# Kernel tuning notes

Measured on AMD Instinct MI355X. Metric: run time of the kernel, lower is better.

## Reference

```python
import jax, jax.numpy as jnp
import numpy as np

B, S, VOCAB, HID, NCLS = 64, 512, 1400, 256, 128


def _time_lstm(W_all, b_all, U_all, b_u, W_d, b_d, x, ts):
    # x: [b, s, h], ts: [b, s]
    b = x.shape[0]
    h0 = jnp.zeros((b, HID), x.dtype)
    c0 = jnp.zeros((b, HID), x.dtype)

    def step(carry, xt):
        h, c = carry
        x_t, t_t = xt  # [b,h], [b]
        c_s1 = jnp.tanh(c @ W_d.T + b_d)
        c_adj = (c - c_s1) + c_s1 * t_t[:, None]
        gates = jax.nn.sigmoid(h @ W_all.T + b_all + x_t @ U_all.T + b_u)
        f, i, o, c_tmp = jnp.split(gates, 4, axis=1)  # note: c_tmp is sigmoid, as in source
        c_new = f * c_adj + i * c_tmp
        h_new = o * jnp.tanh(c_new)
        return (h_new, c_new), h_new

    _, hs = jax.lax.scan(step, (h0, c0), (x.transpose(1, 0, 2), ts.T))
    return hs.transpose(1, 0, 2)  # [b, s, h]


def setup_inputs() -> dict:
    key = jax.random.key(0)
    ks = jax.random.split(key, 18)

    def g(k, shape, scale=0.05):
        return jax.random.normal(k, shape, dtype=jnp.float32) * scale

    return {
        "inputs": jax.random.uniform(ks[0], (B, S, VOCAB), dtype=jnp.float32),
        "timestamps": jax.random.uniform(ks[1], (B, S), dtype=jnp.float32),
        "emb": g(ks[2], (VOCAB, HID)),
        "W_all1": g(ks[3], (4 * HID, HID)), "b_all1": g(ks[4], (4 * HID,)),
        "U_all1": g(ks[5], (4 * HID, HID)), "b_u1": g(ks[6], (4 * HID,)),
        "W_d1": g(ks[7], (HID, HID)), "b_d1": g(ks[8], (HID,)),
        "W_all2": g(ks[9], (4 * HID, HID)), "b_all2": g(ks[10], (4 * HID,)),
        "U_all2": g(ks[11], (4 * HID, HID)), "b_u2": g(ks[12], (4 * HID,)),
        "W_d2": g(ks[13], (HID, HID)), "b_d2": g(ks[14], (HID,)),
        "wa": g(ks[15], (1, HID)),
        "Wb": g(ks[16], (HID, HID)),
        "W_out": g(ks[17], (NCLS, HID)),
    }


def reference(inputs, timestamps, emb, W_all1, b_all1, U_all1, b_u1, W_d1, b_d1,
              W_all2, b_all2, U_all2, b_u2, W_d2, b_d2, wa, Wb, W_out):
    embedded = jnp.einsum('bsv,vh->bsh', inputs, emb)  # multi-hot embedding lookup
    out1 = _time_lstm(W_all1, b_all1, U_all1, b_u1, W_d1, b_d1, embedded, timestamps)
    out2 = _time_lstm(W_all2, b_all2, U_all2, b_u2, W_d2, b_d2, embedded, timestamps)
    alpha = jax.nn.softmax(jnp.einsum('bsh,oh->bs', out1, wa), axis=1)  # [b,s]
    Beta = jnp.tanh(jnp.einsum('bsh,gh->bsg', out2, Wb))  # [b,s,h]
    ctx = jnp.sum(embedded * Beta * alpha[:, :, None], axis=1)  # [b,h]
    return ctx @ W_out.T  # [b, num_classes]
```

## Files before the change

kernel.cpp:

```cpp
#include <hip/hip_runtime.h>

typedef __attribute__((ext_vector_type(8))) short short8;
typedef __attribute__((ext_vector_type(4))) float f32x4;

#define B_   64
#define S_   512
#define V_   1400
#define VP_  1408
#define H_   256
#define G4_  1024
#define NC_  128
#define CH_  64

__device__ __forceinline__ unsigned short f2bf(float f) {
    unsigned u = __builtin_bit_cast(unsigned, f);
    u += 0x7FFFu + ((u >> 16) & 1u);
    return (unsigned short)(u >> 16);
}
__device__ __forceinline__ float bf2f(unsigned short h) {
    unsigned u = ((unsigned)h) << 16;
    return __builtin_bit_cast(float, u);
}
__device__ __forceinline__ float fsig(float x) {
    x = fminf(fmaxf(x, -40.f), 40.f);
    float e = __builtin_amdgcn_exp2f(x * -1.44269504f);
    return __builtin_amdgcn_rcpf(1.0f + e);
}
__device__ __forceinline__ float ftanh(float x) {
    x = fminf(fmaxf(x, -40.f), 40.f);
    float e = __builtin_amdgcn_exp2f(x * 2.88539008f);
    return 1.0f - 2.0f * __builtin_amdgcn_rcpf(e + 1.0f);
}

__device__ __forceinline__ short8 gload16_sc1(const unsigned short* p) {
    short8 r;
    asm volatile("global_load_dwordx4 %0, %1, off sc1"
                 : "=v"(r) : "v"((unsigned long long)p));
    return r;
}
__device__ __forceinline__ void gstore_short_sc1(unsigned short* p, unsigned v) {
    asm volatile("global_store_short %0, %1, off sc1"
                 :: "v"((unsigned long long)p), "v"(v));
}

__global__ void k0_prep(const float* __restrict__ emb,
                        const float* __restrict__ Wa1, const float* __restrict__ Wa2,
                        const float* __restrict__ Wd1, const float* __restrict__ Wd2,
                        const float* __restrict__ U1,  const float* __restrict__ U2,
                        const float* __restrict__ ba1, const float* __restrict__ bu1,
                        const float* __restrict__ ba2, const float* __restrict__ bu2,
                        const float* __restrict__ Wb,
                        unsigned short* __restrict__ embT, unsigned short* __restrict__ Wg,
                        unsigned short* __restrict__ Wd,   unsigned short* __restrict__ Ub,
                        unsigned short* __restrict__ Wbb,  float* __restrict__ bg,
                        unsigned int* __restrict__ cnt) {
    int tid = blockIdx.x * blockDim.x + threadIdx.x;
    int np = gridDim.x * blockDim.x;
    for (int i = tid; i < 256 * VP_; i += np) {
        int n = i / VP_, k = i - n * VP_;
        embT[i] = (k < V_) ? f2bf(emb[k * H_ + n]) : (unsigned short)0;
    }
    for (int i = tid; i < G4_ * H_; i += np) {
        Wg[i] = f2bf(Wa1[i]); Wg[G4_ * H_ + i] = f2bf(Wa2[i]);
        Ub[i] = f2bf(U1[i]);  Ub[G4_ * H_ + i] = f2bf(U2[i]);
    }
    for (int i = tid; i < H_ * H_; i += np) {
        Wd[i] = f2bf(Wd1[i]); Wd[H_ * H_ + i] = f2bf(Wd2[i]); Wbb[i] = f2bf(Wb[i]);
    }
    for (int i = tid; i < G4_; i += np) {
        bg[i] = ba1[i] + bu1[i]; bg[G4_ + i] = ba2[i] + bu2[i];
    }
    for (int i = tid; i < 512; i += np) cnt[i] = 0;
}

__global__ __launch_bounds__(512, 2) void k1_embed(const float* __restrict__ inputs,
                                                   const unsigned short* __restrict__ embT,
                                                   unsigned short* __restrict__ embB) {
    const int tid = threadIdx.x;
    const int w = tid >> 6, ln = tid & 63, q = ln >> 4, l16 = ln & 15;
    const int mt = w >> 2, ng = (w & 3) * 4;
    const int Rbase = blockIdx.x * 32 + mt * 16;
    const float* arow = inputs + (long)(Rbase + l16) * V_;

    f32x4 acc[4];
    #pragma unroll
    for (int i = 0; i < 4; ++i) acc[i] = (f32x4){0.f, 0.f, 0.f, 0.f};

    for (int kt = 0; kt < 44; ++kt) {
        int k0 = kt * 32 + q * 8;
        short8 af;
        if (kt == 43 && q == 3) {
            #pragma unroll
            for (int j = 0; j < 8; ++j) af[j] = 0;
        } else {
            f32x4 x0 = *(const f32x4*)(arow + k0);
            f32x4 x1 = *(const f32x4*)(arow + k0 + 4);
            #pragma unroll
            for (int j = 0; j < 4; ++j) { af[j] = (short)f2bf(x0[j]); af[4 + j] = (short)f2bf(x1[j]); }
        }
        #pragma unroll
        for (int i = 0; i < 4; ++i) {
            short8 bf = *(const short8*)(embT + (long)((ng + i) * 16 + l16) * VP_ + k0);
            acc[i] = __builtin_amdgcn_mfma_f32_16x16x32_bf16(af, bf, acc[i], 0, 0, 0);
        }
    }
    #pragma unroll
    for (int i = 0; i < 4; ++i) {
        int col = (ng + i) * 16 + l16;
        #pragma unroll
        for (int j = 0; j < 4; ++j) {
            int R = Rbase + 4 * q + j;
            embB[(long)R * H_ + col] = f2bf(acc[i][j]);
        }
    }
}

__global__ __launch_bounds__(512, 2) void k2_pre(const unsigned short* __restrict__ embB,
                                                 const unsigned short* __restrict__ Ub,
                                                 const float* __restrict__ bg,
                                                 float* __restrict__ P, int t0) {
    const int tid = threadIdx.x;
    const int w = tid >> 6, ln = tid & 63, q = ln >> 4, l16 = ln & 15;
    const int rbase = blockIdx.x * 32;

    short8 af[2][8];
    #pragma unroll
    for (int mt = 0; mt < 2; ++mt)
        #pragma unroll
        for (int kt = 0; kt < 8; ++kt) {
            int rp = rbase + mt * 16 + l16;
            int rg = t0 * 64 + rp;
            int b = rg & 63, s = rg >> 6;
            af[mt][kt] = *(const short8*)(embB + ((long)b * S_ + s) * H_ + kt * 32 + q * 8);
        }

    for (int i = 0; i < 16; ++i) {
        int nt2 = w * 16 + i;
        int l = nt2 >> 6;
        int gcol = (nt2 & 63) * 16 + l16;
        float bias = bg[nt2 * 16 + l16];
        short8 bf[8];
        #pragma unroll
        for (int kt = 0; kt < 8; ++kt)
            bf[kt] = *(const short8*)(Ub + (long)(nt2 * 16 + l16) * H_ + kt * 32 + q * 8);
        #pragma unroll
        for (int mt = 0; mt < 2; ++mt) {
            f32x4 acc = (f32x4){bias, bias, bias, bias};
            #pragma unroll
            for (int kt = 0; kt < 8; ++kt)
                acc = __builtin_amdgcn_mfma_f32_16x16x32_bf16(af[mt][kt], bf[kt], acc, 0, 0, 0);
            int rp0 = rbase + mt * 16;
            float* dst = P + ((long)l * (CH_ * 64) + rp0 + 4 * q) * G4_ + gcol;
            #pragma unroll
            for (int j = 0; j < 4; ++j) dst[(long)j * G4_] = acc[j];
        }
    }
}

__global__ __launch_bounds__(256, 1) void k3_lstm(const float* __restrict__ ts,
                                                  const unsigned short* __restrict__ W,
                                                  const float* __restrict__ bd1,
                                                  const float* __restrict__ bd2,
                                                  const float* __restrict__ P,
                                                  unsigned short* __restrict__ out1,
                                                  unsigned short* __restrict__ out2,
                                                  float* __restrict__ cst,
                                                  unsigned short* __restrict__ cx,
                                                  unsigned int* __restrict__ cnt,
                                                  int t0) {
    __shared__ float ts_lds[16][CH_];

    const int tid = threadIdx.x;
    const int w = tid >> 6, ln = tid & 63, q = ln >> 4, l16 = ln & 15;
    const int bid = blockIdx.x;
    const int l = bid >> 4, m = (bid >> 2) & 3, cg = bid & 3;
    const int b0 = m * 16;
    const int hc0 = cg * 64 + w * 16;
    const int mycol = hc0 + l16;
    const int cidx = (l * 4 + m) * 64;
    unsigned short* outp = l ? out2 : out1;
    const float bdv = (l ? bd2 : bd1)[mycol];

    for (int i = tid; i < 16 * CH_; i += 256) {
        int r = i >> 6, cc = i & (CH_ - 1);
        ts_lds[r][cc] = ts[(b0 + r) * S_ + t0 + cc];
    }

    short8 wg[4][8];
    short8 wd[8];
    #pragma unroll
    for (int g = 0; g < 4; ++g)
        #pragma unroll
        for (int kt = 0; kt < 8; ++kt)
            wg[g][kt] = *(const short8*)(W + ((long)(l * G4_ + g * H_ + mycol)) * H_ + kt * 32 + q * 8);
    #pragma unroll
    for (int kt = 0; kt < 8; ++kt)
        wd[kt] = *(const short8*)(W + (long)2 * G4_ * H_ + ((long)(l * H_ + mycol)) * H_ + kt * 32 + q * 8);

    #pragma unroll
    for (int g = 0; g < 4; ++g)
        #pragma unroll
        for (int kt = 0; kt < 8; ++kt)
            asm volatile("" : "+v"(wg[g][kt]));
    #pragma unroll
    for (int kt = 0; kt < 8; ++kt)
        asm volatile("" : "+v"(wd[kt]));

    float cf[4];
    if (t0 == 0) {
        cf[0] = cf[1] = cf[2] = cf[3] = 0.f;
    } else {
        #pragma unroll
        for (int j = 0; j < 4; ++j)
            cf[j] = cst[(long)(l * 4 + m) * 4096 + (4 * q + j) * 256 + mycol];
    }
    __syncthreads();

    const float* Pbase = P + ((long)l * (CH_ * 64) + b0) * G4_;

    #pragma unroll 1
    for (int t = 0; t < CH_; ++t) {
        const int gt = t0 + t;

        float pv[4][4];
        #pragma unroll
        for (int g = 0; g < 4; ++g)
            #pragma unroll
            for (int j = 0; j < 4; ++j)
                pv[g][j] = Pbase[((long)t * 64 + 4 * q + j) * G4_ + g * H_ + mycol];
        asm volatile("" ::: "memory");

        {
            unsigned target = 4u * (unsigned)gt;
            while (__hip_atomic_load(&cnt[cidx], __ATOMIC_RELAXED, __HIP_MEMORY_SCOPE_AGENT) < target)
                __builtin_amdgcn_s_sleep(1);
        }

        short8 ha[8], ca[8];
        if (gt == 0) {
            #pragma unroll
            for (int kt = 0; kt < 8; ++kt) {
                #pragma unroll
                for (int j = 0; j < 8; ++j) { ha[kt][j] = 0; ca[kt][j] = 0; }
            }
        } else {
            const unsigned short* crow = cx + ((long)(((gt - 1) & 1) * 8 + l * 4 + m)) * 4096 + l16 * 256 + q * 8;
            const unsigned short* hrow = outp + ((long)(b0 + l16) * S_ + (gt - 1)) * H_ + q * 8;
            #pragma unroll
            for (int kt = 0; kt < 8; ++kt) ca[kt] = gload16_sc1(crow + kt * 32);
            #pragma unroll
            for (int kt = 0; kt < 8; ++kt) ha[kt] = gload16_sc1(hrow + kt * 32);
        }
        asm volatile("s_waitcnt vmcnt(8)" ::: "memory");
        __builtin_amdgcn_sched_barrier(0);

        f32x4 dacc = (f32x4){bdv, bdv, bdv, bdv};
        #pragma unroll
        for (int kt = 0; kt < 8; ++kt)
            dacc = __builtin_amdgcn_mfma_f32_16x16x32_bf16(ca[kt], wd[kt], dacc, 0, 0, 0);

        asm volatile("s_waitcnt vmcnt(0)" ::: "memory");
        __builtin_amdgcn_sched_barrier(0);

        f32x4 gacc[4];
        #pragma unroll
        for (int g = 0; g < 4; ++g) {
            gacc[g] = (f32x4){pv[g][0], pv[g][1], pv[g][2], pv[g][3]};
            #pragma unroll
            for (int kt = 0; kt < 8; ++kt)
                gacc[g] = __builtin_amdgcn_mfma_f32_16x16x32_bf16(ha[kt], wg[g][kt], gacc[g], 0, 0, 0);
        }

        #pragma unroll
        for (int j = 0; j < 4; ++j) {
            int r = 4 * q + j;
            float tv = ts_lds[r][t];
            float cs1 = ftanh(dacc[j]);
            float cadj = cf[j] + cs1 * (tv - 1.0f);
            float fg = fsig(gacc[0][j]), ig = fsig(gacc[1][j]);
            float og = fsig(gacc[2][j]), ct = fsig(gacc[3][j]);
            float cn = fg * cadj + ig * ct;
            float hn = og * ftanh(cn);
            cf[j] = cn;
            gstore_short_sc1(outp + ((long)(b0 + r) * S_ + gt) * H_ + mycol, (unsigned)f2bf(hn));
            gstore_short_sc1(cx + ((long)((gt & 1) * 8 + l * 4 + m)) * 4096 + r * 256 + mycol, (unsigned)f2bf(cn));
        }

        asm volatile("s_waitcnt vmcnt(0)" ::: "memory");
        __syncthreads();
        if (tid == 0) atomicAdd(&cnt[cidx], 1u);
    }

    #pragma unroll
    for (int j = 0; j < 4; ++j)
        cst[(long)(l * 4 + m) * 4096 + (4 * q + j) * 256 + mycol] = cf[j];
}

__global__ __launch_bounds__(512) void k4a_alpha(const unsigned short* __restrict__ out1,
                                                 const float* __restrict__ wa,
                                                 float* __restrict__ alpha) {
    __shared__ float sc[512];
    __shared__ float red[512];
    const int b = blockIdx.x, tid = threadIdx.x;
    const int w = tid >> 6, ln = tid & 63;
    f32x4 wv = *(const f32x4*)(wa + ln * 4);
    for (int i = 0; i < 64; ++i) {
        int s = w * 64 + i;
        const unsigned short* row = out1 + ((long)b * S_ + s) * H_ + ln * 4;
        float d = bf2f(row[0]) * wv[0] + bf2f(row[1]) * wv[1] +
                  bf2f(row[2]) * wv[2] + bf2f(row[3]) * wv[3];
        #pragma unroll
        for (int off = 32; off; off >>= 1) d += __shfl_xor(d, off);
        if (ln == 0) sc[s] = d;
    }
    __syncthreads();
    float v = sc[tid];
    red[tid] = v;
    for (int st = 256; st; st >>= 1) {
        __syncthreads();
        if (tid < st) red[tid] = fmaxf(red[tid], red[tid + st]);
    }
    __syncthreads();
    float M = red[0];
    __syncthreads();
    float e = __builtin_amdgcn_exp2f((v - M) * 1.44269504f);
    red[tid] = e;
    for (int st = 256; st; st >>= 1) {
        __syncthreads();
        if (tid < st) red[tid] += red[tid + st];
    }
    __syncthreads();
    alpha[b * S_ + tid] = e * __builtin_amdgcn_rcpf(red[0]);
}

__global__ __launch_bounds__(512, 2) void k4b_ctx(const unsigned short* __restrict__ out2,
                                                  const unsigned short* __restrict__ Wbb,
                                                  const unsigned short* __restrict__ embB,
                                                  const float* __restrict__ alpha,
                                                  float* __restrict__ ctx) {
    __shared__ float cbuf[32][256];
    const int b = blockIdx.x, tid = threadIdx.x;
    const int w = tid >> 6, ln = tid & 63, q = ln >> 4, l16 = ln & 15;

    float cp[16];
    #pragma unroll
    for (int nt = 0; nt < 16; ++nt) cp[nt] = 0.f;

    for (int i = 0; i < 4; ++i) {
        int mt = w * 4 + i;
        short8 af[8];
        #pragma unroll
        for (int kt = 0; kt < 8; ++kt)
            af[kt] = *(const short8*)(out2 + ((long)b * S_ + mt * 16 + l16) * H_ + kt * 32 + q * 8);
        float al[4];
        #pragma unroll
        for (int j = 0; j < 4; ++j) al[j] = alpha[b * S_ + mt * 16 + 4 * q + j];
        for (int nt = 0; nt < 16; ++nt) {
            f32x4 acc = (f32x4){0.f, 0.f, 0.f, 0.f};
            #pragma unroll
            for (int kt = 0; kt < 8; ++kt) {
                short8 bf = *(const short8*)(Wbb + (long)(nt * 16 + l16) * H_ + kt * 32 + q * 8);
                acc = __builtin_amdgcn_mfma_f32_16x16x32_bf16(af[kt], bf, acc, 0, 0, 0);
            }
            #pragma unroll
            for (int j = 0; j < 4; ++j) {
                int s = mt * 16 + 4 * q + j;
                float beta = ftanh(acc[j]);
                float ev = bf2f(embB[((long)b * S_ + s) * H_ + nt * 16 + l16]);
                cp[nt] += beta * al[j] * ev;
            }
        }
    }
    #pragma unroll
    for (int nt = 0; nt < 16; ++nt) cbuf[w * 4 + q][nt * 16 + l16] = cp[nt];
    __syncthreads();
    if (tid < 256) {
        float sum = 0.f;
        for (int i = 0; i < 32; ++i) sum += cbuf[i][tid];
        ctx[b * H_ + tid] = sum;
    }
}

__global__ void k4c_out(const float* __restrict__ ctx, const float* __restrict__ Wout,
                        float* __restrict__ out) {
    int b = blockIdx.x, n = threadIdx.x;
    const f32x4* cr = (const f32x4*)(ctx + b * H_);
    const f32x4* wr = (const f32x4*)(Wout + n * H_);
    float acc = 0.f;
    #pragma unroll 8
    for (int i = 0; i < 64; ++i) {
        f32x4 c = cr[i], ww = wr[i];
        acc += c[0] * ww[0] + c[1] * ww[1] + c[2] * ww[2] + c[3] * ww[3];
    }
    out[b * NC_ + n] = acc;
}

extern "C" void kernel_launch(void* const* d_in, const int* in_sizes, int n_in,
                              void* d_out, int out_size, void* d_ws, size_t ws_size,
                              hipStream_t stream) {
    (void)in_sizes; (void)n_in; (void)out_size; (void)ws_size;
    const float* inputs = (const float*)d_in[0];
    const float* tsp    = (const float*)d_in[1];
    const float* emb    = (const float*)d_in[2];
    const float* Wa1 = (const float*)d_in[3];  const float* ba1 = (const float*)d_in[4];
    const float* U1  = (const float*)d_in[5];  const float* bu1 = (const float*)d_in[6];
    const float* Wd1 = (const float*)d_in[7];  const float* bd1 = (const float*)d_in[8];
    const float* Wa2 = (const float*)d_in[9];  const float* ba2 = (const float*)d_in[10];
    const float* U2  = (const float*)d_in[11]; const float* bu2 = (const float*)d_in[12];
    const float* Wd2 = (const float*)d_in[13]; const float* bd2 = (const float*)d_in[14];
    const float* wa  = (const float*)d_in[15];
    const float* Wb  = (const float*)d_in[16];
    const float* Wout = (const float*)d_in[17];
    float* out = (float*)d_out;

    char* ws = (char*)d_ws;
    unsigned short* embT = (unsigned short*)(ws + 0);
    unsigned short* Wg   = (unsigned short*)(ws + 720896);
    unsigned short* Wd   = (unsigned short*)(ws + 1769472);
    unsigned short* Ub   = (unsigned short*)(ws + 2031616);
    unsigned short* Wbb  = (unsigned short*)(ws + 3080192);
    float*          bgp  = (float*)(ws + 3211264);
    unsigned short* embB = (unsigned short*)(ws + 3219456);
    float*          P    = (float*)(ws + 19996672);
    unsigned short* out1 = (unsigned short*)(ws + 53551104);
    unsigned short* out2 = (unsigned short*)(ws + 70328320);
    unsigned short* cx   = (unsigned short*)(ws + 87105536);
    float*          cst  = (float*)(ws + 87236608);
    float*          alp  = (float*)(ws + 87367680);
    float*          ctx  = (float*)(ws + 87498752);
    unsigned int*   cnt  = (unsigned int*)(ws + 87564288);

    hipLaunchKernelGGL(k0_prep, dim3(256), dim3(256), 0, stream,
                       emb, Wa1, Wa2, Wd1, Wd2, U1, U2, ba1, bu1, ba2, bu2, Wb,
                       embT, Wg, Wd, Ub, Wbb, bgp, cnt);
    hipLaunchKernelGGL(k1_embed, dim3(1024), dim3(512), 0, stream, inputs, embT, embB);
    for (int c = 0; c < 8; ++c) {
        hipLaunchKernelGGL(k2_pre, dim3(128), dim3(512), 0, stream, embB, Ub, bgp, P, c * CH_);
        hipLaunchKernelGGL(k3_lstm, dim3(32), dim3(256), 0, stream, tsp, Wg, bd1, bd2, P,
                           out1, out2, cst, cx, cnt, c * CH_);
    }
    hipLaunchKernelGGL(k4a_alpha, dim3(64), dim3(512), 0, stream, out1, wa, alp);
    hipLaunchKernelGGL(k4b_ctx, dim3(64), dim3(512), 0, stream, out2, Wbb, embB, alp, ctx);
    hipLaunchKernelGGL(k4c_out, dim3(64), dim3(128), 0, stream, ctx, Wout, out);
}
```

Before: 2.983 ms.

## Overlap next-chunk input projection with LSTM recurrence and interleave two batch groups

The recurrent kernel now also computes the input-gate projection for the next time chunk in extra blocks, writing into a double-buffered P array, so the projection no longer runs serially between recurrence launches. Each recurrent block now handles two independent batch groups whose steps are interleaved, hiding one chain's memory latency behind the other. Synchronisation changes from a per-block barrier counter to per-wave polling of per-chunk counters, which has an iteration cap. Adding P to the accumulator moves from before the MFMA chain to after it. The projection blocks may contend with the latency-critical recurrence blocks for memory bandwidth, and the fused path needs a larger workspace, with a fallback when it is too small.

```diff
diff --git a/kernel.cpp b/kernel.cpp
--- a/kernel.cpp
+++ b/kernel.cpp
@@ -35,13 +35,21 @@
 __device__ __forceinline__ short8 gload16_sc1(const unsigned short* p) {
     short8 r;
     asm volatile("global_load_dwordx4 %0, %1, off sc1"
-                 : "=v"(r) : "v"((unsigned long long)p));
+                 : "=&v"(r) : "v"((unsigned long long)p));
     return r;
 }
 __device__ __forceinline__ void gstore_short_sc1(unsigned short* p, unsigned v) {
     asm volatile("global_store_short %0, %1, off sc1"
                  :: "v"((unsigned long long)p), "v"(v));
 }
+__device__ __forceinline__ float gloadf_plain(const float* p) {
+    float r;
+    asm volatile("global_load_dword %0, %1, off"
+                 : "=&v"(r) : "v"((unsigned long long)p));
+    return r;
+}
+
+#define CNT_ZONE_ 4096
 
 __global__ void k0_prep(const float* __restrict__ emb,
                         const float* __restrict__ Wa1, const float* __restrict__ Wa2,
@@ -70,7 +78,7 @@
     for (int i = tid; i < G4_; i += np) {
         bg[i] = ba1[i] + bu1[i]; bg[G4_ + i] = ba2[i] + bu2[i];
     }
-    for (int i = tid; i < 512; i += np) cnt[i] = 0;
+    for (int i = tid; i < CNT_ZONE_; i += np) cnt[i] = 0;
 }
 
 __global__ __launch_bounds__(512, 2) void k1_embed(const float* __restrict__ inputs,
@@ -157,33 +165,84 @@
     }
 }
 
-__global__ __launch_bounds__(256, 1) void k3_lstm(const float* __restrict__ ts,
-                                                  const unsigned short* __restrict__ W,
-                                                  const float* __restrict__ bd1,
-                                                  const float* __restrict__ bd2,
-                                                  const float* __restrict__ P,
-                                                  unsigned short* __restrict__ out1,
-                                                  unsigned short* __restrict__ out2,
-                                                  float* __restrict__ cst,
-                                                  unsigned short* __restrict__ cx,
-                                                  unsigned int* __restrict__ cnt,
-                                                  int t0) {
-    __shared__ float ts_lds[16][CH_];
-
+__global__ __launch_bounds__(256, 1) void k3_fused(const float* __restrict__ ts,
+                                                   const unsigned short* __restrict__ W,
+                                                   const float* __restrict__ bd1,
+                                                   const float* __restrict__ bd2,
+                                                   const float* __restrict__ Pcur,
+                                                   unsigned short* __restrict__ out1,
+                                                   unsigned short* __restrict__ out2,
+                                                   float* __restrict__ cst,
+                                                   unsigned short* __restrict__ cx,
+                                                   unsigned int* __restrict__ cnt,
+                                                   int t0,
+                                                   const unsigned short* __restrict__ embB,
+                                                   const unsigned short* __restrict__ Ub,
+                                                   const float* __restrict__ bg,
+                                                   float* __restrict__ Pnext,
+                                                   int next_t0) {
     const int tid = threadIdx.x;
     const int w = tid >> 6, ln = tid & 63, q = ln >> 4, l16 = ln & 15;
     const int bid = blockIdx.x;
-    const int l = bid >> 4, m = (bid >> 2) & 3, cg = bid & 3;
-    const int b0 = m * 16;
+
+    if (bid >= 16) {
+        const int g2 = bid - 16;
+        const int rbase = (g2 >> 1) * 32;
+        const int hb = g2 & 1;
+
+        short8 af[2][8];
+        #pragma unroll
+        for (int mt = 0; mt < 2; ++mt)
+            #pragma unroll
+            for (int kt = 0; kt < 8; ++kt) {
+                int rp = rbase + mt * 16 + l16;
+                int rg = next_t0 * 64 + rp;
+                int b = rg & 63, s = rg >> 6;
+                af[mt][kt] = *(const short8*)(embB + ((long)b * S_ + s) * H_ + kt * 32 + q * 8);
+            }
+
+        for (int i = 0; i < 16; ++i) {
+            int nt2 = hb * 64 + w * 16 + i;
+            int l = nt2 >> 6;
+            int gcol = (nt2 & 63) * 16 + l16;
+            float bias = bg[nt2 * 16 + l16];
+            short8 bf[8];
+            #pragma unroll
+            for (int kt = 0; kt < 8; ++kt)
+                bf[kt] = *(const short8*)(Ub + (long)(nt2 * 16 + l16) * H_ + kt * 32 + q * 8);
+            #pragma unroll
+            for (int mt = 0; mt < 2; ++mt) {
+                f32x4 acc = (f32x4){bias, bias, bias, bias};
+                #pragma unroll
+                for (int kt = 0; kt < 8; ++kt)
+                    acc = __builtin_amdgcn_mfma_f32_16x16x32_bf16(af[mt][kt], bf[kt], acc, 0, 0, 0);
+                int rp0 = rbase + mt * 16;
+                float* dst = Pnext + ((long)l * (CH_ * 64) + rp0 + 4 * q) * G4_ + gcol;
+                #pragma unroll
+                for (int j = 0; j < 4; ++j) dst[(long)j * G4_] = acc[j];
+            }
+        }
+        return;
+    }
+
+    __shared__ float ts_lds[2][16][CH_];
+    const int chunk = t0 >> 6;
+
+    const int l = bid >> 3, mp = (bid >> 2) & 1, cg = bid & 3;
+    const int mA = mp, mB = mp + 2;
+    const int grpA = l * 4 + mA, grpB = l * 4 + mB;
+    const int b0A = mA * 16, b0B = mB * 16;
     const int hc0 = cg * 64 + w * 16;
     const int mycol = hc0 + l16;
-    const int cidx = (l * 4 + m) * 64;
+    unsigned int* cellA = cnt + (chunk * 8 + grpA) * 64;
+    unsigned int* cellB = cnt + (chunk * 8 + grpB) * 64;
     unsigned short* outp = l ? out2 : out1;
     const float bdv = (l ? bd2 : bd1)[mycol];
 
-    for (int i = tid; i < 16 * CH_; i += 256) {
-        int r = i >> 6, cc = i & (CH_ - 1);
-        ts_lds[r][cc] = ts[(b0 + r) * S_ + t0 + cc];
+    for (int i = tid; i < 2 * 16 * CH_; i += 256) {
+        int ch = i >> 10, r = (i >> 6) & 15, cc = i & (CH_ - 1);
+        int b0 = (ch ? b0B : b0A);
+        ts_lds[ch][r][cc] = ts[(b0 + r) * S_ + t0 + cc];
     }
 
     short8 wg[4][8];
@@ -197,103 +256,115 @@
     for (int kt = 0; kt < 8; ++kt)
         wd[kt] = *(const short8*)(W + (long)2 * G4_ * H_ + ((long)(l * H_ + mycol)) * H_ + kt * 32 + q * 8);
 
-    #pragma unroll
-    for (int g = 0; g < 4; ++g)
+    float cfA[4], cfB[4];
+    if (t0 == 0) {
+        #pragma unroll
+        for (int j = 0; j < 4; ++j) { cfA[j] = 0.f; cfB[j] = 0.f; }
+    } else {
+        #pragma unroll
+        for (int j = 0; j < 4; ++j) {
+            cfA[j] = cst[(long)grpA * 4096 + (4 * q + j) * 256 + mycol];
+            cfB[j] = cst[(long)grpB * 4096 + (4 * q + j) * 256 + mycol];
+        }
+    }
+    __syncthreads();
+
+    const float* PbA = Pcur + ((long)l * (CH_ * 64) + b0A) * G4_;
+    const float* PbB = Pcur + ((long)l * (CH_ * 64) + b0B) * G4_;
+    unsigned opaque_zero;
+    asm volatile("v_mov_b32 %0, 0" : "=v"(opaque_zero));
+
+    auto chain_step = [&](int t, int gt, int b0, int grp, unsigned int* cell,
+                          float (&cf)[4], const float (*tsrow)[CH_], const float* PbC) {
+        if (t) {
+            const unsigned tgt = 16u * (unsigned)t;
+            unsigned it = 0;
+            for (;;) {
+                unsigned v = 0;
+                if (ln == 0)
+                    v = __hip_atomic_fetch_add(cell, opaque_zero,
+                                               __ATOMIC_RELAXED, __HIP_MEMORY_SCOPE_AGENT);
+                v = __shfl(v, 0);
+                if (v >= tgt || ++it >= (1u << 14)) break;
+            }
+        }
+        __builtin_amdgcn_sched_barrier(0);
+
+        short8 ha[8], ca[8];
+        if (gt == 0) {
+            #pragma unroll
+            for (int kt = 0; kt < 8; ++kt) {
+                #pragma unroll
+                for (int jj = 0; jj < 8; ++jj) { ha[kt][jj] = 0; ca[kt][jj] = 0; }
+            }
+        } else {
+            const unsigned short* crow = cx + ((long)(((gt - 1) & 1) * 8 + grp)) * 4096 + l16 * 256 + q * 8;
+            const unsigned short* hrow = outp + ((long)(b0 + l16) * S_ + (gt - 1)) * H_ + q * 8;
+            #pragma unroll
+            for (int kt = 0; kt < 8; ++kt) ca[kt] = gload16_sc1(crow + kt * 32);
+            #pragma unroll
+            for (int kt = 0; kt < 8; ++kt) ha[kt] = gload16_sc1(hrow + kt * 32);
+        }
+        float pv[4][4];
+        #pragma unroll
+        for (int g = 0; g < 4; ++g)
+            #pragma unroll
+            for (int j = 0; j < 4; ++j)
+                pv[g][j] = gloadf_plain(PbC + ((long)t * 64 + 4 * q + j) * G4_ + g * H_ + mycol);
+
+        asm volatile("s_waitcnt vmcnt(24)" ::: "memory");
+        __builtin_amdgcn_sched_barrier(0);
+        f32x4 dacc = (f32x4){bdv, bdv, bdv, bdv};
         #pragma unroll
         for (int kt = 0; kt < 8; ++kt)
-            asm volatile("" : "+v"(wg[g][kt]));
-    #pragma unroll
-    for (int kt = 0; kt < 8; ++kt)
-        asm volatile("" : "+v"(wd[kt]));
-
-    float cf[4];
-    if (t0 == 0) {
-        cf[0] = cf[1] = cf[2] = cf[3] = 0.f;
-    } else {
-        #pragma unroll
-        for (int j = 0; j < 4; ++j)
-            cf[j] = cst[(long)(l * 4 + m) * 4096 + (4 * q + j) * 256 + mycol];
-    }
-    __syncthreads();
-
-    const float* Pbase = P + ((long)l * (CH_ * 64) + b0) * G4_;
+            dacc = __builtin_amdgcn_mfma_f32_16x16x32_bf16(ca[kt], wd[kt], dacc, 0, 0, 0);
+
+        asm volatile("s_waitcnt vmcnt(16)" ::: "memory");
+        __builtin_amdgcn_sched_barrier(0);
+        f32x4 gacc[4];
+        #pragma unroll
+        for (int g = 0; g < 4; ++g) {
+            gacc[g] = (f32x4){0.f, 0.f, 0.f, 0.f};
+            #pragma unroll
+            for (int kt = 0; kt < 8; ++kt)
+                gacc[g] = __builtin_amdgcn_mfma_f32_16x16x32_bf16(ha[kt], wg[g][kt], gacc[g], 0, 0, 0);
+        }
+
+        asm volatile("s_waitcnt vmcnt(0)" ::: "memory");
+        __builtin_amdgcn_sched_barrier(0);
+        #pragma unroll
+        for (int j = 0; j < 4; ++j) {
+            int r = 4 * q + j;
+            float tv = tsrow[r][t];
+            float cs1 = ftanh(dacc[j]);
+            float cadj = cf[j] + cs1 * (tv - 1.0f);
+            float fg = fsig(gacc[0][j] + pv[0][j]);
+            float ig = fsig(gacc[1][j] + pv[1][j]);
+            float og = fsig(gacc[2][j] + pv[2][j]);
+            float cg2 = fsig(gacc[3][j] + pv[3][j]);
+            float cn = fg * cadj + ig * cg2;
+            float hn = og * ftanh(cn);
+            cf[j] = cn;
+            gstore_short_sc1(outp + ((long)(b0 + r) * S_ + gt) * H_ + mycol, (unsigned)f2bf(hn));
+            gstore_short_sc1(cx + ((long)((gt & 1) * 8 + grp)) * 4096 + r * 256 + mycol, (unsigned)f2bf(cn));
+        }
+        asm volatile("s_waitcnt vmcnt(0)" ::: "memory");
+        if (ln == 0)
+            (void)__hip_atomic_fetch_add(cell, 1u, __ATOMIC_RELAXED, __HIP_MEMORY_SCOPE_AGENT);
+    };
 
     #pragma unroll 1
     for (int t = 0; t < CH_; ++t) {
         const int gt = t0 + t;
-
-        float pv[4][4];
-        #pragma unroll
-        for (int g = 0; g < 4; ++g)
-            #pragma unroll
-            for (int j = 0; j < 4; ++j)
-                pv[g][j] = Pbase[((long)t * 64 + 4 * q + j) * G4_ + g * H_ + mycol];
-        asm volatile("" ::: "memory");
-
-        {
-            unsigned target = 4u * (unsigned)gt;
-            while (__hip_atomic_load(&cnt[cidx], __ATOMIC_RELAXED, __HIP_MEMORY_SCOPE_AGENT) < target)
-                __builtin_amdgcn_s_sleep(1);
-        }
-
-        short8 ha[8], ca[8];
-        if (gt == 0) {
-            #pragma unroll
-            for (int kt = 0; kt < 8; ++kt) {
-                #pragma unroll
-                for (int j = 0; j < 8; ++j) { ha[kt][j] = 0; ca[kt][j] = 0; }
-            }
-        } else {
-            const unsigned short* crow = cx + ((long)(((gt - 1) & 1) * 8 + l * 4 + m)) * 4096 + l16 * 256 + q * 8;
-            const unsigned short* hrow = outp + ((long)(b0 + l16) * S_ + (gt - 1)) * H_ + q * 8;
-            #pragma unroll
-            for (int kt = 0; kt < 8; ++kt) ca[kt] = gload16_sc1(crow + kt * 32);
-            #pragma unroll
-            for (int kt = 0; kt < 8; ++kt) ha[kt] = gload16_sc1(hrow + kt * 32);
-        }
-        asm volatile("s_waitcnt vmcnt(8)" ::: "memory");
-        __builtin_amdgcn_sched_barrier(0);
-
-        f32x4 dacc = (f32x4){bdv, bdv, bdv, bdv};
-        #pragma unroll
-        for (int kt = 0; kt < 8; ++kt)
-            dacc = __builtin_amdgcn_mfma_f32_16x16x32_bf16(ca[kt], wd[kt], dacc, 0, 0, 0);
-
-        asm volatile("s_waitcnt vmcnt(0)" ::: "memory");
-        __builtin_amdgcn_sched_barrier(0);
-
-        f32x4 gacc[4];
-        #pragma unroll
-        for (int g = 0; g < 4; ++g) {
-            gacc[g] = (f32x4){pv[g][0], pv[g][1], pv[g][2], pv[g][3]};
-            #pragma unroll
-            for (int kt = 0; kt < 8; ++kt)
-                gacc[g] = __builtin_amdgcn_mfma_f32_16x16x32_bf16(ha[kt], wg[g][kt], gacc[g], 0, 0, 0);
-        }
-
-        #pragma unroll
-        for (int j = 0; j < 4; ++j) {
-            int r = 4 * q + j;
-            float tv = ts_lds[r][t];
-            float cs1 = ftanh(dacc[j]);
-            float cadj = cf[j] + cs1 * (tv - 1.0f);
-            float fg = fsig(gacc[0][j]), ig = fsig(gacc[1][j]);
-            float og = fsig(gacc[2][j]), ct = fsig(gacc[3][j]);
-            float cn = fg * cadj + ig * ct;
-            float hn = og * ftanh(cn);
-            cf[j] = cn;
-            gstore_short_sc1(outp + ((long)(b0 + r) * S_ + gt) * H_ + mycol, (unsigned)f2bf(hn));
-            gstore_short_sc1(cx + ((long)((gt & 1) * 8 + l * 4 + m)) * 4096 + r * 256 + mycol, (unsigned)f2bf(cn));
-        }
-
-        asm volatile("s_waitcnt vmcnt(0)" ::: "memory");
-        __syncthreads();
-        if (tid == 0) atomicAdd(&cnt[cidx], 1u);
-    }
-
-    #pragma unroll
-    for (int j = 0; j < 4; ++j)
-        cst[(long)(l * 4 + m) * 4096 + (4 * q + j) * 256 + mycol] = cf[j];
+        chain_step(t, gt, b0A, grpA, cellA, cfA, ts_lds[0], PbA);
+        chain_step(t, gt, b0B, grpB, cellB, cfB, ts_lds[1], PbB);
+    }
+
+    #pragma unroll
+    for (int j = 0; j < 4; ++j) {
+        cst[(long)grpA * 4096 + (4 * q + j) * 256 + mycol] = cfA[j];
+        cst[(long)grpB * 4096 + (4 * q + j) * 256 + mycol] = cfB[j];
+    }
 }
 
 __global__ __launch_bounds__(512) void k4a_alpha(const unsigned short* __restrict__ out1,
@@ -398,7 +469,7 @@
 extern "C" void kernel_launch(void* const* d_in, const int* in_sizes, int n_in,
                               void* d_out, int out_size, void* d_ws, size_t ws_size,
                               hipStream_t stream) {
-    (void)in_sizes; (void)n_in; (void)out_size; (void)ws_size;
+    (void)in_sizes; (void)n_in; (void)out_size;
     const float* inputs = (const float*)d_in[0];
     const float* tsp    = (const float*)d_in[1];
     const float* emb    = (const float*)d_in[2];
@@ -421,7 +492,7 @@
     unsigned short* Wbb  = (unsigned short*)(ws + 3080192);
     float*          bgp  = (float*)(ws + 3211264);
     unsigned short* embB = (unsigned short*)(ws + 3219456);
-    float*          P    = (float*)(ws + 19996672);
+    float*          P0   = (float*)(ws + 19996672);
     unsigned short* out1 = (unsigned short*)(ws + 53551104);
     unsigned short* out2 = (unsigned short*)(ws + 70328320);
     unsigned short* cx   = (unsigned short*)(ws + 87105536);
@@ -429,15 +500,30 @@
     float*          alp  = (float*)(ws + 87367680);
     float*          ctx  = (float*)(ws + 87498752);
     unsigned int*   cnt  = (unsigned int*)(ws + 87564288);
+    float*          P1   = (float*)(ws + 87719936);
+    const size_t NEED_FUSED = 121274368;
+    const bool fuse = (ws_size >= NEED_FUSED);
 
     hipLaunchKernelGGL(k0_prep, dim3(256), dim3(256), 0, stream,
                        emb, Wa1, Wa2, Wd1, Wd2, U1, U2, ba1, bu1, ba2, bu2, Wb,
                        embT, Wg, Wd, Ub, Wbb, bgp, cnt);
     hipLaunchKernelGGL(k1_embed, dim3(1024), dim3(512), 0, stream, inputs, embT, embB);
+    hipLaunchKernelGGL(k2_pre, dim3(128), dim3(512), 0, stream, embB, Ub, bgp, P0, 0);
+
+    float* Pb[2] = { P0, fuse ? P1 : P0 };
     for (int c = 0; c < 8; ++c) {
-        hipLaunchKernelGGL(k2_pre, dim3(128), dim3(512), 0, stream, embB, Ub, bgp, P, c * CH_);
-        hipLaunchKernelGGL(k3_lstm, dim3(32), dim3(256), 0, stream, tsp, Wg, bd1, bd2, P,
-                           out1, out2, cst, cx, cnt, c * CH_);
+        if (fuse) {
+            int ng = (c < 7) ? 256 : 0;
+            hipLaunchKernelGGL(k3_fused, dim3(16 + ng), dim3(256), 0, stream,
+                               tsp, Wg, bd1, bd2, Pb[c & 1], out1, out2, cst, cx, cnt, c * CH_,
+                               embB, Ub, bgp, Pb[(c + 1) & 1], (c + 1) * CH_);
+        } else {
+            if (c > 0)
+                hipLaunchKernelGGL(k2_pre, dim3(128), dim3(512), 0, stream, embB, Ub, bgp, P0, c * CH_);
+            hipLaunchKernelGGL(k3_fused, dim3(16), dim3(256), 0, stream,
+                               tsp, Wg, bd1, bd2, P0, out1, out2, cst, cx, cnt, c * CH_,
+                               embB, Ub, bgp, P0, S_ );
+        }
     }
     hipLaunchKernelGGL(k4a_alpha, dim3(64), dim3(512), 0, stream, out1, wa, alp);
     hipLaunchKernelGGL(k4b_ctx, dim3(64), dim3(512), 0, stream, out2, Wbb, embB, alp, ctx);
```

Measured after the change: 4.598 ms. 1.54x slower.
